# Optimization experiments

Measured on AMD Instinct MI355X. Metric: run time of the kernel, lower is better.

## Reference

```python
import jax, jax.numpy as jnp
import numpy as np

IN, H, B, T = 64, 256, 128, 512

def _uniform(key, shape, std):
    return jax.random.uniform(key, shape, jnp.float32, -std, std)

def setup_inputs() -> dict:
    key = jax.random.key(0)
    ks = jax.random.split(key, 16)
    std = 1.0 / np.sqrt(H)
    inp = {
        'x': jax.random.normal(ks[0], (B, T, IN), jnp.float32),
        # layer 1 sLSTM cell
        'Wxh1': _uniform(ks[1], (4 * H, IN), std), 'bxh1': _uniform(ks[2], (4 * H,), std),
        'Whh1': _uniform(ks[3], (4 * H, H), std),  'bhh1': _uniform(ks[4], (4 * H,), std),
        # layer 2 sLSTM cell
        'Wxh2': _uniform(ks[5], (4 * H, H), std),  'bxh2': _uniform(ks[6], (4 * H,), std),
        'Whh2': _uniform(ks[7], (4 * H, H), std),  'bhh2': _uniform(ks[8], (4 * H,), std),
        # head MLP
        'W1': _uniform(ks[9], (H // 2, H), 1.0 / np.sqrt(H)),      'b1': _uniform(ks[10], (H // 2,), 1.0 / np.sqrt(H)),
        'W2': _uniform(ks[11], (H // 4, H // 2), 1.0 / np.sqrt(H // 2)), 'b2': _uniform(ks[12], (H // 4,), 1.0 / np.sqrt(H // 2)),
        'W3': _uniform(ks[13], (1, H // 4), 1.0 / np.sqrt(H // 4)),      'b3': _uniform(ks[14], (1,), 1.0 / np.sqrt(H // 4)),
    }
    return inp

def _slstm_cell(x, h, c, m, n, Wxh, bxh, Whh, bhh):
    # gates: [B, 4H]
    gates = x @ Wxh.T + bxh + h @ Whh.T + bhh
    ig, fg, zg, og = jnp.split(gates, 4, axis=1)
    z_t = jnp.tanh(zg)
    o_t = jax.nn.sigmoid(og)
    # stabilizer: log(exp(fg)) = fg, log(exp(ig)) = ig
    m_t = jnp.maximum(fg + m, ig)
    i_t = jnp.exp(ig - m_t)
    f_t = jnp.exp(fg + m - m_t)
    c_t = f_t * c + i_t * z_t
    n_t = f_t * n + i_t
    h_t = o_t * (c_t / n_t)
    return h_t, c_t, m_t, n_t

def reference(x, Wxh1, bxh1, Whh1, bhh1, Wxh2, bxh2, Whh2, bhh2, W1, b1, W2, b2, W3, b3):
    Bq = x.shape[0]
    z = jnp.zeros((Bq, H), x.dtype)
    init = (z, z, z, z, z, z, z, z)  # (h1,c1,m1,n1,h2,c2,m2,n2)

    def step(carry, x_t):
        h1, c1, m1, n1, h2, c2, m2, n2 = carry
        h1, c1, m1, n1 = _slstm_cell(x_t, h1, c1, m1, n1, Wxh1, bxh1, Whh1, bhh1)
        h2, c2, m2, n2 = _slstm_cell(h1, h2, c2, m2, n2, Wxh2, bxh2, Whh2, bhh2)
        return (h1, c1, m1, n1, h2, c2, m2, n2), None

    carry, _ = jax.lax.scan(step, init, jnp.swapaxes(x, 0, 1))  # scan over time
    out = carry[4]  # last h2 == outputs[:, -1, :]
    out = jax.nn.relu(out @ W1.T + b1)   # dropout is identity in eval
    out = jax.nn.relu(out @ W2.T + b2)
    out = out @ W3.T + b3
    return out.squeeze(-1)  # [B]
```

## Files before the change

kernel.cpp:

```cpp
#include <hip/hip_runtime.h>
#include <stdint.h>

typedef unsigned short ushort_t;
typedef __attribute__((ext_vector_type(8))) short short8;
typedef __attribute__((ext_vector_type(4))) float float4v;
typedef __attribute__((ext_vector_type(4))) int int4v;

#define TSTEPS 512
#define NBATCH 128
#define HID 256
#define NIN 64
#define RB 32
#define NBHID (NBATCH*HID)
#define RING_DW (RB*NBHID)

#define OFF_FLAGS   0u
#define OFF_BIAS    16384u
#define OFF_H1R     32768u
#define RING_BYTES  (RB*(unsigned)NBATCH*HID*4u)
#define OFF_H2R     (OFF_H1R + RING_BYTES)
#define OFF_H1F     (OFF_H2R + RING_BYTES)
#define OFF_H2F     (OFF_H1F + RING_BYTES)
#define OFF_WF1     (OFF_H2F + RING_BYTES)
#define WF1_FRAGS   (16*8*4*4)
#define OFF_WF2     (OFF_WF1 + WF1_FRAGS*1024u)
#define WF2_FRAGS   (16*8*6*4)
#define OFF_HOUT    (OFF_WF2 + WF2_FRAGS*1024u)


__device__ __forceinline__ ushort_t bf16h(float f) {
    unsigned u = __float_as_uint(f);
    u += 0x7fffu + ((u >> 16) & 1u);
    return (ushort_t)(u >> 16);
}
__device__ __forceinline__ float bf16f(ushort_t h) {
    return __uint_as_float(((unsigned)h) << 16);
}
__device__ __forceinline__ unsigned genbit(int s) {
    return ((unsigned)(s + 64) >> 5) & 1u;
}


template<bool SYS>
__device__ __forceinline__ int ld_i32(const void* p) {
    int r;
    if constexpr (SYS)
        asm volatile("global_load_dword %0, %1, off sc0 sc1\n\ts_waitcnt vmcnt(0)"
                     : "=v"(r) : "v"(p) : "memory");
    else
        asm volatile("global_load_dword %0, %1, off sc0\n\ts_waitcnt vmcnt(0)"
                     : "=v"(r) : "v"(p) : "memory");
    return r;
}
__device__ __forceinline__ float ld_cg_f32(const void* p) {
    float r;
    asm volatile("global_load_dword %0, %1, off sc0 sc1\n\ts_waitcnt vmcnt(0)"
                 : "=v"(r) : "v"(p) : "memory");
    return r;
}
template<bool SYS>
__device__ __forceinline__ void ld2x4(int4v& a, int4v& b, const void* p) {
    if constexpr (SYS)
        asm volatile("global_load_dwordx4 %0, %2, off sc0 sc1\n\t"
                     "global_load_dwordx4 %1, %2, off offset:16 sc0 sc1\n\t"
                     "s_waitcnt vmcnt(0)"
                     : "=&v"(a), "=&v"(b) : "v"(p) : "memory");
    else
        asm volatile("global_load_dwordx4 %0, %2, off sc0\n\t"
                     "global_load_dwordx4 %1, %2, off offset:16 sc0\n\t"
                     "s_waitcnt vmcnt(0)"
                     : "=&v"(a), "=&v"(b) : "v"(p) : "memory");
}
template<bool SYS>
__device__ __forceinline__ void ld4x4(int4v& a, int4v& b, int4v& c, int4v& d,
                                      const void* p, const void* q) {
    if constexpr (SYS)
        asm volatile("global_load_dwordx4 %0, %4, off sc0 sc1\n\t"
                     "global_load_dwordx4 %1, %4, off offset:16 sc0 sc1\n\t"
                     "global_load_dwordx4 %2, %5, off sc0 sc1\n\t"
                     "global_load_dwordx4 %3, %5, off offset:16 sc0 sc1\n\t"
                     "s_waitcnt vmcnt(0)"
                     : "=&v"(a), "=&v"(b), "=&v"(c), "=&v"(d)
                     : "v"(p), "v"(q) : "memory");
    else
        asm volatile("global_load_dwordx4 %0, %4, off sc0\n\t"
                     "global_load_dwordx4 %1, %4, off offset:16 sc0\n\t"
                     "global_load_dwordx4 %2, %5, off sc0\n\t"
                     "global_load_dwordx4 %3, %5, off offset:16 sc0\n\t"
                     "s_waitcnt vmcnt(0)"
                     : "=&v"(a), "=&v"(b), "=&v"(c), "=&v"(d)
                     : "v"(p), "v"(q) : "memory");
}
__device__ __forceinline__ void st_u32_fast(void* p, unsigned v) {
    asm volatile("global_store_dword %0, %1, off sc0" :: "v"(p), "v"(v) : "memory");
}
__device__ __forceinline__ void st_u32_safe(void* p, unsigned v) {
    asm volatile("global_store_dword %0, %1, off sc0 sc1" :: "v"(p), "v"(v) : "memory");
}
__device__ __forceinline__ void st_cg_i32(int* p, int v) {
    asm volatile("global_store_dword %0, %1, off sc0 sc1" :: "v"(p), "v"(v) : "memory");
}
__device__ __forceinline__ void st_cg_f32(void* p, float v) {
    asm volatile("global_store_dword %0, %1, off sc0 sc1" :: "v"(p), "v"(v) : "memory");
}

__device__ __forceinline__ bool tag8(int4v a, int4v b, unsigned gw) {
    unsigned x = ((unsigned)a[0] ^ gw) | ((unsigned)a[1] ^ gw) |
                 ((unsigned)a[2] ^ gw) | ((unsigned)a[3] ^ gw) |
                 ((unsigned)b[0] ^ gw) | ((unsigned)b[1] ^ gw) |
                 ((unsigned)b[2] ^ gw) | ((unsigned)b[3] ^ gw);
    return (x & 1u) == 0u;
}

__device__ __forceinline__ int4v ext_hi8(int4v a, int4v b) {
    int4v r;
    r[0] = (int)__builtin_amdgcn_perm((unsigned)a[1], (unsigned)a[0], 0x05040100u);
    r[1] = (int)__builtin_amdgcn_perm((unsigned)a[3], (unsigned)a[2], 0x05040100u);
    r[2] = (int)__builtin_amdgcn_perm((unsigned)b[1], (unsigned)b[0], 0x05040100u);
    r[3] = (int)__builtin_amdgcn_perm((unsigned)b[3], (unsigned)b[2], 0x05040100u);
    return r;
}
__device__ __forceinline__ int4v ext_lo8(int4v a, int4v b) {
    int4v r;
    r[0] = (int)__builtin_amdgcn_perm((unsigned)a[1], (unsigned)a[0], 0x07060302u);
    r[1] = (int)__builtin_amdgcn_perm((unsigned)a[3], (unsigned)a[2], 0x07060302u);
    r[2] = (int)__builtin_amdgcn_perm((unsigned)b[1], (unsigned)b[0], 0x07060302u);
    r[3] = (int)__builtin_amdgcn_perm((unsigned)b[3], (unsigned)b[2], 0x07060302u);
    return r;
}


__global__ void prep_misc(const float* bxh1, const float* bhh1,
                          const float* bxh2, const float* bhh2,
                          float* bias, int* flags, unsigned* ring_all)
{
    int n = blockIdx.x * blockDim.x + threadIdx.x;
    if (n < 1024)       bias[n] = bxh1[n] + bhh1[n];
    else if (n < 2048)  bias[n] = bxh2[n - 1024] + bhh2[n - 1024];
    else if (n < 6144)  flags[n - 2048] = 0;
    else {
        unsigned d = n - 6144;
        if (d < 4u * RING_DW)
            ring_all[d] = 0x00000001u;
    }
}

__global__ void prep_wf(const float* Wxh1, const float* Whh1,
                        const float* Wxh2, const float* Whh2,
                        ushort_t* wf1, ushort_t* wf2)
{
    int n = blockIdx.x * blockDim.x + threadIdx.x;
    const int L1E = WF1_FRAGS * 512;
    const int L2E = WF2_FRAGS * 512;
    if (n >= L1E + L2E) return;
    int layer = (n >= L1E) ? 1 : 0;
    int e = layer ? (n - L1E) : n;
    int el = e & 511;
    int f  = e >> 9;
    int lane = el >> 3, j = el & 7;
    int nt = f & 3;
    int rem = f >> 2;
    int i, wv, slice, F, S;
    if (!layer) { F = 4; S = 10; i = rem & 3; wv = (rem >> 2) & 7; slice = rem >> 5; }
    else        { F = 6; S = 16; i = rem % 6; int r2 = rem / 6; wv = r2 & 7; slice = r2 >> 3; }
    int fg = wv * F + i;
    int col = lane & 15;
    int row = nt * 256 + slice * 16 + col;
    float val = 0.f;
    if (fg < 3 * S) {
        int sec = (fg < S) ? 0 : ((fg < 2 * S) ? 1 : 2);
        int ks = (fg - sec * S) * 32 + (lane >> 4) * 8 + j;
        float w;
        if (!layer) w = (ks < 256) ? Whh1[row * 256 + ks] : Wxh1[row * 64 + (ks - 256)];
        else        w = (ks < 256) ? Wxh2[row * 256 + ks] : Whh2[row * 256 + (ks - 256)];
        ushort_t hi = bf16h(w);
        val = (sec < 2) ? bf16f(hi) : (w - bf16f(hi));
    }
    (layer ? wf2 : wf1)[e] = bf16h(val);
}


template<int LAYER, int F, int S, int PITCH>
__device__ __forceinline__ void run_layer(
    int g, int slice, int tid, const float* __restrict__ x,
    int* flags, const float* bias,
    unsigned* h1r, unsigned* h2r, unsigned* h1f, unsigned* h2f,
    const ushort_t* wfrag, float* hOut,
    ushort_t* sA, ushort_t* sB, float (*red)[4][64][4], int* fastMode)
{
    const int wv = tid >> 6, lane = tid & 63;
    const int mrow = lane & 15, q = lane >> 4;
    int* f1 = flags + g * 256;
    int* f2 = flags + 2048 + g * 256;
    int* myflag = flags + LAYER * 2048 + g * 256 + slice * 16;

    short8 bw[4][F];
    {
        const ushort_t* base = wfrag + (size_t)((slice * 8 + wv) * F) * 4 * 512;
        #pragma unroll
        for (int i = 0; i < F; i++)
            #pragma unroll
            for (int nt = 0; nt < 4; nt++)
                bw[nt][i] = *(const short8*)(base + (i * 4 + nt) * 512 + lane * 8);
    }

    float bs[4];
    #pragma unroll
    for (int nt = 0; nt < 4; nt++)
        bs[nt] = bias[LAYER * 1024 + nt * 256 + slice * 16 + mrow];

    float cst[4] = {0,0,0,0}, mst[4] = {0,0,0,0}, nst[4] = {0,0,0,0};

    const int sr = tid >> 5, k = tid & 31;
    const int row = g * 16 + sr;

    if (tid == 0) *fastMode = 1;
    __syncthreads();

    for (int t = 0; t < TSTEPS; t++) {
        if (LAYER == 0 && tid >= 128 && tid < 256) {
            int idx = tid - 128;
            int r = idx >> 3, o = idx & 7;
            const float* xsrc = x + ((size_t)(g * 16 + r) * TSTEPS + t) * NIN + o * 8;
            float4v x0 = *(const float4v*)xsrc;
            float4v x1 = *(const float4v*)(xsrc + 4);
            float xs[8] = {x0[0], x0[1], x0[2], x0[3], x1[0], x1[1], x1[2], x1[3]};
            union { ushort_t u[8]; int4v v4; } hiP, loP;
            #pragma unroll
            for (int z = 0; z < 8; z++) {
                ushort_t hi = bf16h(xs[z]);
                hiP.u[z] = hi;
                loP.u[z] = bf16h(xs[z] - bf16f(hi));
            }
            *(int4v*)(sA + r * PITCH + (32 + o) * 8) = hiP.v4;
            *(int4v*)(sB + r * PITCH + (32 + o) * 8) = loP.v4;
        }

        if (tid >= 64 && tid < 128) {
            int pl = tid - 64;
            const unsigned *spF = nullptr, *spS = nullptr;
            unsigned want = 0;
            if (LAYER == 0) {
                if (pl < 16) {
                    size_t off = (size_t)((t - 1) & (RB - 1)) * NBHID
                               + (size_t)(g * 16 + 15) * HID + pl * 16 + 15;
                    spF = h1f + off; spS = h1r + off; want = genbit(t - 1);
                }
            } else {
                if (pl < 16) {
                    size_t off = (size_t)(t & (RB - 1)) * NBHID
                               + (size_t)(g * 16 + 15) * HID + pl * 16 + 15;
                    spF = h1f + off; spS = h1r + off; want = genbit(t);
                } else if (pl < 32) {
                    size_t off = (size_t)((t - 1) & (RB - 1)) * NBHID
                               + (size_t)(g * 16 + 15) * HID + (pl - 16) * 16 + 15;
                    spF = h2f + off; spS = h2r + off; want = genbit(t - 1);
                }
            }
            if (spF) {
                if (*fastMode) {
                    bool ok = false;
                    for (int it = 0; it < 256; it++) {
                        if ((((unsigned)ld_i32<false>(spF)) & 1u) == want) { ok = true; break; }
                    }
                    if (!ok) {
                        *fastMode = 0;
                        while ((((unsigned)ld_i32<true>(spS)) & 1u) != want) { }
                    }
                } else {
                    while ((((unsigned)ld_i32<true>(spS)) & 1u) != want) { }
                }
            } else if (pl >= 32 && (t & 7) == 0) {
                int thr = t - 22;
                const int* p = nullptr;
                if (LAYER == 0) {
                    if (pl < 48)      p = f1 + (pl - 32) * 16;
                    else              p = f2 + (pl - 48) * 16;
                } else {
                    if (pl < 48)      p = f2 + (pl - 32) * 16;
                }
                if (p)
                    while (ld_i32<true>(p) < thr) { }
            }
        }
        __syncthreads();

        {
            const bool fm = (*fastMode != 0);
            if (LAYER == 0) {
                size_t off = ((size_t)((t - 1) & (RB - 1)) * NBATCH + row) * HID + k * 8;
                unsigned w = genbit(t - 1);
                int4v a, b;
                bool ok = false;
                if (fm) {
                    for (int it = 0; it < 32; it++) {
                        ld2x4<false>(a, b, h1f + off);
                        if (tag8(a, b, w)) { ok = true; break; }
                    }
                }
                if (!ok) {
                    if (fm) *fastMode = 0;
                    do { ld2x4<true>(a, b, h1r + off); } while (!tag8(a, b, w));
                }
                *(int4v*)(sA + sr * PITCH + k * 8) = ext_hi8(a, b);
                *(int4v*)(sB + sr * PITCH + k * 8) = ext_lo8(a, b);
            } else {
                size_t off1 = ((size_t)(t & (RB - 1)) * NBATCH + row) * HID + k * 8;
                size_t off2 = ((size_t)((t - 1) & (RB - 1)) * NBATCH + row) * HID + k * 8;
                unsigned w1 = genbit(t), w2 = genbit(t - 1);
                int4v a, b, c, d;
                bool ok = false;
                if (fm) {
                    for (int it = 0; it < 32; it++) {
                        ld4x4<false>(a, b, c, d, h1f + off1, h2f + off2);
                        if (tag8(a, b, w1) && tag8(c, d, w2)) { ok = true; break; }
                    }
                }
                if (!ok) {
                    if (fm) *fastMode = 0;
                    do { ld4x4<true>(a, b, c, d, h1r + off1, h2r + off2); }
                    while (!(tag8(a, b, w1) && tag8(c, d, w2)));
                }
                *(int4v*)(sA + sr * PITCH + k * 8)        = ext_hi8(a, b);
                *(int4v*)(sB + sr * PITCH + k * 8)        = ext_lo8(a, b);
                *(int4v*)(sA + sr * PITCH + (32 + k) * 8) = ext_hi8(c, d);
                *(int4v*)(sB + sr * PITCH + (32 + k) * 8) = ext_lo8(c, d);
            }
        }
        __syncthreads();

        if (tid == 256 && (t & 7) == 0)
            st_cg_i32(myflag, t);

        float4v acc[4] = {};
        #pragma unroll
        for (int i = 0; i < F; i++) {
            const int fg = wv * F + i;
            short8 a;
            if (fg < 3 * S) {
                int sec = (fg >= S && fg < 2 * S) ? 1 : 0;
                int ks = ((fg < S) ? fg : ((fg < 2 * S) ? fg - S : fg - 2 * S)) * 32;
                const ushort_t* ap = (sec ? sB : sA) + mrow * PITCH + ks + q * 8;
                a = *(const short8*)ap;
            } else {
                a = (short8){0,0,0,0,0,0,0,0};
            }
            #pragma unroll
            for (int nt = 0; nt < 4; nt++)
                acc[nt] = __builtin_amdgcn_mfma_f32_16x16x32_bf16(a, bw[nt][i], acc[nt], 0, 0, 0);
        }

        if (wv != 0) {
            #pragma unroll
            for (int nt = 0; nt < 4; nt++) *(float4v*)red[wv - 1][nt][lane] = acc[nt];
        }
        __syncthreads();

        if (wv == 0) {
            #pragma unroll
            for (int w = 0; w < 7; w++)
                #pragma unroll
                for (int nt = 0; nt < 4; nt++)
                    acc[nt] += *(const float4v*)red[w][nt][lane];

            unsigned* baseS = (LAYER ? h2r : h1r) + (size_t)(t & (RB - 1)) * NBHID;
            unsigned* baseF = (LAYER ? h2f : h1f) + (size_t)(t & (RB - 1)) * NBHID;
            unsigned gw = genbit(t);
            #pragma unroll
            for (int r2 = 0; r2 < 4; r2++) {
                float ig  = acc[0][r2] + bs[0];
                float fgt = acc[1][r2] + bs[1];
                float zg  = acc[2][r2] + bs[2];
                float og  = acc[3][r2] + bs[3];
                float zc = fminf(fmaxf(zg, -15.f), 15.f);
                float e2 = __expf(2.f * zc);
                float zt = (e2 - 1.f) / (e2 + 1.f);
                float ot = 1.f / (1.f + __expf(-og));
                float mt = fmaxf(fgt + mst[r2], ig);
                float it = __expf(ig - mt);
                float ft = __expf(fgt + mst[r2] - mt);
                cst[r2] = ft * cst[r2] + it * zt;
                nst[r2] = ft * nst[r2] + it;
                mst[r2] = mt;
                float h = ot * (cst[r2] / nst[r2]);
                ushort_t hi = (ushort_t)(((unsigned)bf16h(h) & 0xFFFEu) | gw);
                float rem = h - bf16f(hi);
                ushort_t lo = bf16h(rem);
                unsigned word = ((unsigned)lo << 16) | (unsigned)hi;
                int orow = g * 16 + q * 4 + r2;
                int col = slice * 16 + mrow;
                size_t idx = (size_t)orow * HID + col;
                st_u32_fast(baseF + idx, word);
                st_u32_safe(baseS + idx, word);
                if (LAYER == 1 && t == TSTEPS - 1)
                    st_cg_f32(hOut + idx, h);
            }
        }
    }
}

__global__ __launch_bounds__(512, 2) void recur(
    const float* __restrict__ x,
    int* flags, const float* bias,
    unsigned* h1r, unsigned* h2r, unsigned* h1f, unsigned* h2f,
    const ushort_t* wf1, const ushort_t* wf2, float* hOut)
{
    __shared__ alignas(16) ushort_t sA[16 * 520];
    __shared__ alignas(16) ushort_t sB[16 * 520];
    __shared__ float red[7][4][64][4];
    __shared__ int fastMode;
    int g = blockIdx.x & 7;
    int loc = blockIdx.x >> 3;
    if (loc < 16)
        run_layer<0, 4, 10, 328>(g, loc, threadIdx.x, x, flags, bias,
                                 h1r, h2r, h1f, h2f, wf1, hOut, sA, sB, red, &fastMode);
    else
        run_layer<1, 6, 16, 520>(g, loc - 16, threadIdx.x, x, flags, bias,
                                 h1r, h2r, h1f, h2f, wf2, hOut, sA, sB, red, &fastMode);
}


__global__ void head_mlp(const float* hOut, const float* W1, const float* b1,
                         const float* W2, const float* b2, const float* W3, const float* b3,
                         float* out)
{
    __shared__ float h[256];
    __shared__ float a1[128];
    __shared__ float a2[64];
    int b = blockIdx.x, j = threadIdx.x;
    for (int k = j; k < 256; k += 128)
        h[k] = ld_cg_f32(hOut + (size_t)b * HID + k);
    __syncthreads();
    float s = b1[j];
    for (int k = 0; k < 256; k++) s += W1[j * 256 + k] * h[k];
    a1[j] = fmaxf(s, 0.f);
    __syncthreads();
    if (j < 64) {
        float s2 = b2[j];
        for (int k = 0; k < 128; k++) s2 += W2[j * 128 + k] * a1[k];
        a2[j] = fmaxf(s2, 0.f);
    }
    __syncthreads();
    if (j == 0) {
        float s3 = b3[0];
        for (int k = 0; k < 64; k++) s3 += W3[k] * a2[k];
        out[b] = s3;
    }
}


extern "C" void kernel_launch(void* const* d_in, const int* in_sizes, int n_in,
                              void* d_out, int out_size, void* d_ws, size_t ws_size,
                              hipStream_t stream)
{
    const float* x    = (const float*)d_in[0];
    const float* Wxh1 = (const float*)d_in[1];
    const float* bxh1 = (const float*)d_in[2];
    const float* Whh1 = (const float*)d_in[3];
    const float* bhh1 = (const float*)d_in[4];
    const float* Wxh2 = (const float*)d_in[5];
    const float* bxh2 = (const float*)d_in[6];
    const float* Whh2 = (const float*)d_in[7];
    const float* bhh2 = (const float*)d_in[8];
    const float* W1   = (const float*)d_in[9];
    const float* b1   = (const float*)d_in[10];
    const float* W2   = (const float*)d_in[11];
    const float* b2   = (const float*)d_in[12];
    const float* W3   = (const float*)d_in[13];
    const float* b3   = (const float*)d_in[14];

    char* w = (char*)d_ws;
    int*      flags = (int*)(w + OFF_FLAGS);
    float*    bias  = (float*)(w + OFF_BIAS);
    unsigned* h1r   = (unsigned*)(w + OFF_H1R);
    unsigned* h2r   = (unsigned*)(w + OFF_H2R);
    unsigned* h1f   = (unsigned*)(w + OFF_H1F);
    unsigned* h2f   = (unsigned*)(w + OFF_H2F);
    ushort_t* wf1   = (ushort_t*)(w + OFF_WF1);
    ushort_t* wf2   = (ushort_t*)(w + OFF_WF2);
    float*    hOut  = (float*)(w + OFF_HOUT);

    prep_misc<<<(6144 + 4 * RING_DW + 255) / 256, 256, 0, stream>>>(
        bxh1, bhh1, bxh2, bhh2, bias, flags, h1r);
    prep_wf<<<((WF1_FRAGS + WF2_FRAGS) * 512 + 255) / 256, 256, 0, stream>>>(
        Wxh1, Whh1, Wxh2, Whh2, wf1, wf2);

    const float* xp = x;
    void* args[] = { (void*)&xp, (void*)&flags, (void*)&bias,
                     (void*)&h1r, (void*)&h2r, (void*)&h1f, (void*)&h2f,
                     (void*)&wf1, (void*)&wf2, (void*)&hOut };
    hipLaunchCooperativeKernel((void*)recur, dim3(256), dim3(512), args, 0, stream);

    head_mlp<<<NBATCH, 128, 0, stream>>>(hOut, W1, b1, W2, b2, W3, b3, (float*)d_out);
}
```

Measured before the change: 1.912 ms.

## Assign recurrent block roles by XCC so each batch group stays on one die

Each block reads its hardware XCC id and publishes it to a shared table in global memory. After all 256 blocks have published, every block computes the same assignment: blocks on the same XCC form one batch group of 32 (16 per layer), and overflow blocks fill the remaining slots. Fast mode is enabled only for groups that sit entirely on one XCC. The aim is to keep the per-step flag and ring traffic inside one XCC's L2 instead of crossing dies, at the cost of a startup spin-wait that depends on all blocks being resident at once.

```diff
diff --git a/kernel.cpp b/kernel.cpp
--- a/kernel.cpp
+++ b/kernel.cpp
@@ -26,6 +26,7 @@
 #define OFF_WF2     (OFF_WF1 + WF1_FRAGS*1024u)
 #define WF2_FRAGS   (16*8*6*4)
 #define OFF_HOUT    (OFF_WF2 + WF2_FRAGS*1024u)
+
 
 
 __device__ __forceinline__ ushort_t bf16h(float f) {
@@ -137,8 +138,10 @@
     int n = blockIdx.x * blockDim.x + threadIdx.x;
     if (n < 1024)       bias[n] = bxh1[n] + bhh1[n];
     else if (n < 2048)  bias[n] = bxh2[n - 1024] + bhh2[n - 1024];
-    else if (n < 6144)  flags[n - 2048] = 0;
-    else {
+    else if (n < 6144)  {
+        int i = n - 2048;
+        flags[i] = (i >= 3072 && i < 3328) ? -1 : 0;
+    } else {
         unsigned d = n - 6144;
         if (d < 4u * RING_DW)
             ring_all[d] = 0x00000001u;
@@ -182,7 +185,7 @@
 
 template<int LAYER, int F, int S, int PITCH>
 __device__ __forceinline__ void run_layer(
-    int g, int slice, int tid, const float* __restrict__ x,
+    int g, int slice, int tid, int fastInit, const float* __restrict__ x,
     int* flags, const float* bias,
     unsigned* h1r, unsigned* h2r, unsigned* h1f, unsigned* h2f,
     const ushort_t* wfrag, float* hOut,
@@ -214,7 +217,7 @@
     const int sr = tid >> 5, k = tid & 31;
     const int row = g * 16 + sr;
 
-    if (tid == 0) *fastMode = 1;
+    if (tid == 0) *fastMode = fastInit;
     __syncthreads();
 
     for (int t = 0; t < TSTEPS; t++) {
@@ -409,13 +412,58 @@
     __shared__ alignas(16) ushort_t sB[16 * 520];
     __shared__ float red[7][4][64][4];
     __shared__ int fastMode;
-    int g = blockIdx.x & 7;
-    int loc = blockIdx.x >> 3;
+    __shared__ int xsTab[256];
+    __shared__ int asn[3];
+
+    int* xccTab = flags + 3072;
+    if (threadIdx.x == 0) {
+        unsigned xcc = (unsigned)__builtin_amdgcn_s_getreg(63508);
+        st_cg_i32(xccTab + blockIdx.x, (int)(xcc & 7u));
+    }
+    if (threadIdx.x < 256) {
+        int v;
+        do { v = ld_i32<true>(xccTab + threadIdx.x); } while (v == -1);
+        xsTab[threadIdx.x] = v;
+    }
+    __syncthreads();
+    if (threadIdx.x == 0) {
+        int cnt[8] = {0,0,0,0,0,0,0,0};
+        for (int j = 0; j < 256; j++) cnt[xsTab[j]]++;
+        int run[8] = {0,0,0,0,0,0,0,0};
+        int myGrp = -1, myRole = -1, ovK = -1, ovCount = 0;
+        for (int j = 0; j < 256; j++) {
+            int xv = xsTab[j];
+            int r = run[xv]++;
+            if (r < 32) {
+                if (j == (int)blockIdx.x) { myGrp = xv; myRole = r; }
+            } else {
+                if (j == (int)blockIdx.x) ovK = ovCount;
+                ovCount++;
+            }
+        }
+        if (myGrp < 0) {
+            int k2 = 0; bool done = false;
+            for (int gg = 0; gg < 8 && !done; gg++)
+                for (int rr = cnt[gg]; rr < 32 && !done; rr++) {
+                    if (k2 == ovK) { myGrp = gg; myRole = rr; done = true; }
+                    k2++;
+                }
+        }
+        if (myGrp < 0) { myGrp = blockIdx.x & 7; myRole = blockIdx.x >> 3; }
+        asn[0] = myGrp;
+        asn[1] = myRole;
+        asn[2] = (cnt[myGrp] >= 32) ? 1 : 0;
+    }
+    __syncthreads();
+    const int g = asn[0];
+    const int loc = asn[1];
+    const int fastInit = asn[2];
+
     if (loc < 16)
-        run_layer<0, 4, 10, 328>(g, loc, threadIdx.x, x, flags, bias,
+        run_layer<0, 4, 10, 328>(g, loc, threadIdx.x, fastInit, x, flags, bias,
                                  h1r, h2r, h1f, h2f, wf1, hOut, sA, sB, red, &fastMode);
     else
-        run_layer<1, 6, 16, 520>(g, loc - 16, threadIdx.x, x, flags, bias,
+        run_layer<1, 6, 16, 520>(g, loc - 16, threadIdx.x, fastInit, x, flags, bias,
                                  h1r, h2r, h1f, h2f, wf2, hOut, sA, sB, red, &fastMode);
 }
 
```

Result: slower. 2.225 ms (+16.4%).
